# Kernel optimization log

Hardware: AMD Instinct MI355X
Metric: run time of the kernel (lower is better)

The kernel has to match this reference:

```python
import jax, jax.numpy as jnp
import numpy as np

H = 8; C = 128; P_E = 128; P_D = 64
N = 10000; E = 100000; B = 32
NEG_SLOPE = 0.01  # torch.nn.LeakyReLU default


def setup_inputs() -> dict:
    key = jax.random.key(0)
    ks = jax.random.split(key, 20)
    def lin(k, din, dout):
        return jax.random.normal(k, (din, dout), jnp.float32) / np.float32(np.sqrt(din))
    inp = dict(
        x=jax.random.normal(ks[0], (N, P_E), jnp.float32),
        index=jax.random.randint(ks[1], (2, E), 0, N),
        attr=jax.random.normal(ks[2], (E, P_D), jnp.float32),
        batch=jnp.sort(jax.random.randint(ks[3], (N,), 0, B)),
    )
    i = 4
    for l in (1, 2):
        inp[f"Wq{l}"] = lin(ks[i], P_E, H * C); i += 1
        inp[f"bq{l}"] = jnp.zeros((H * C,), jnp.float32)
        inp[f"Wk{l}"] = lin(ks[i], P_E, H * C); i += 1
        inp[f"bk{l}"] = jnp.zeros((H * C,), jnp.float32)
        inp[f"Wv{l}"] = lin(ks[i], P_E, H * C); i += 1
        inp[f"bv{l}"] = jnp.zeros((H * C,), jnp.float32)
        inp[f"We{l}"] = lin(ks[i], P_D, H * C); i += 1  # lin_edge, bias=False in PyG
        inp[f"Wskip{l}"] = lin(ks[i], P_E, P_E); i += 1  # root/skip linear (concat=False)
        inp[f"bskip{l}"] = jnp.zeros((P_E,), jnp.float32)
        inp[f"gnw{l}"] = jnp.ones((P_E,), jnp.float32)   # GraphNorm weight
        inp[f"gnb{l}"] = jnp.zeros((P_E,), jnp.float32)  # GraphNorm bias
        inp[f"gnm{l}"] = jnp.ones((P_E,), jnp.float32)   # GraphNorm mean_scale
    return inp


def transformer_conv(x, src, dst, attr, Wq, bq, Wk, bk, Wv, bv, We, Wskip, bskip):
    # PyG TransformerConv: heads=H, out_channels=C, concat=False, edge_dim=P_D,
    # dropout inactive (eval). Messages flow src=edge_index[0] -> dst=edge_index[1].
    q = (x @ Wq + bq).reshape(N, H, C)
    k = (x @ Wk + bk).reshape(N, H, C)
    v = (x @ Wv + bv).reshape(N, H, C)
    e = (attr @ We).reshape(E, H, C)
    kj = k[src] + e                                                   # [E,H,C]
    alpha = jnp.einsum('ehc,ehc->eh', q[dst], kj) / np.float32(np.sqrt(C))
    # segment softmax over destination node (numerically stable)
    amax = jax.ops.segment_max(alpha, dst, num_segments=N)            # [N,H]
    ex = jnp.exp(alpha - amax[dst])
    denom = jax.ops.segment_sum(ex, dst, num_segments=N)
    w = ex / (denom[dst] + 1e-16)                                     # [E,H]
    msg = (v[src] + e) * w[:, :, None]                                # [E,H,C]
    out = jax.ops.segment_sum(msg, dst, num_segments=N)               # [N,H,C]
    out = out.mean(axis=1)                                            # concat=False -> head mean
    return out + x @ Wskip + bskip                                    # root_weight=True


def graph_norm(x, batch, w, b, ms, eps=1e-5):
    cnt = jnp.maximum(jax.ops.segment_sum(jnp.ones((N,), x.dtype), batch, num_segments=B), 1.0)
    mean = jax.ops.segment_sum(x, batch, num_segments=B) / cnt[:, None]
    out = x - mean[batch] * ms
    var = jax.ops.segment_sum(out * out, batch, num_segments=B) / cnt[:, None]
    return out / jnp.sqrt(var[batch] + eps) * w + b


def reference(x, index, attr, batch,
              Wq1, bq1, Wk1, bk1, Wv1, bv1, We1, Wskip1, bskip1, gnw1, gnb1, gnm1,
              Wq2, bq2, Wk2, bk2, Wv2, bv2, We2, Wskip2, bskip2, gnw2, gnb2, gnm2):
    src, dst = index[0], index[1]
    h = transformer_conv(x, src, dst, attr, Wq1, bq1, Wk1, bk1, Wv1, bv1, We1, Wskip1, bskip1)
    h = jax.nn.leaky_relu(graph_norm(h, batch, gnw1, gnb1, gnm1), NEG_SLOPE)
    h = transformer_conv(h, src, dst, attr, Wq2, bq2, Wk2, bk2, Wv2, bv2, We2, Wskip2, bskip2)
    return jax.nn.leaky_relu(graph_norm(h, batch, gnw2, gnb2, gnm2), NEG_SLOPE)
```

## Files before the change

### kernel.cpp

```cpp
#include <hip/hip_runtime.h>
#include <hip/hip_bf16.h>
#include <math.h>

#define NN 10000
#define NE 100000
#define NB 32

typedef __attribute__((ext_vector_type(8))) short short8;
typedef __attribute__((ext_vector_type(4))) float f32x4;
typedef __attribute__((ext_vector_type(2))) float f32x2;
typedef _Float16 h2 __attribute__((ext_vector_type(2)));

union H8 { short8 s; h2 h[4]; };
union HU { _Float16 h; ushort u; };

__device__ inline ushort f2b(float f) {
  union { float f; unsigned u; } a; a.f = f;
  unsigned r = a.u + 0x7fff + ((a.u >> 16) & 1);
  return (ushort)(r >> 16);
}
__device__ inline float bf2f(ushort u) {
  union { unsigned u; float f; } a; a.u = ((unsigned)u) << 16;
  return a.f;
}
__device__ inline ushort f2h(float f) { HU x; x.h = (_Float16)f; return x.u; }
__device__ inline float h2f(ushort u) { HU x; x.u = u; return (float)x.h; }

__device__ inline float e4m3_sw(unsigned b) {
  unsigned s = b & 0x80, e = (b >> 3) & 15, m = b & 7;
  float v = (e == 0) ? (float)m * (1.f / 512.f) : ldexpf((float)(8 + m), (int)e - 10);
  return s ? -v : v;
}
__device__ inline unsigned f2e4m3_sw(float f) {
  unsigned s = (__float_as_uint(f) >> 24) & 0x80;
  float a = fabsf(f);
  if (a < 0.0009765625f) return s;
  if (a >= 448.f) return s | 0x7e;
  if (a < 0.015625f) {
    int q = (int)rintf(a * 512.f);
    return s | (unsigned)q;
  }
  int e2; frexpf(a, &e2);
  int sh = e2 - 4;
  int M = (int)rintf(ldexpf(a, -sh));
  if (M >= 16) { M >>= 1; sh++; }
  int E = sh + 10;
  if (E > 15) return s | 0x7e;
  return s | (unsigned)((E << 3) | (M - 8));
}

#if defined(__has_builtin)
#if __has_builtin(__builtin_amdgcn_cvt_pk_f32_fp8) && __has_builtin(__builtin_amdgcn_cvt_pk_fp8_f32)
#define HW_FP8 1
#endif
#endif

#ifdef HW_FP8
template <bool HI>
__device__ inline f32x2 dec2(unsigned w) {
  return __builtin_amdgcn_cvt_pk_f32_fp8((int)w, HI);
}
template <bool HI>
__device__ inline unsigned enc2(float a, float b, unsigned old) {
  return (unsigned)__builtin_amdgcn_cvt_pk_fp8_f32(a, b, (int)old, HI);
}
#else
template <bool HI>
__device__ inline f32x2 dec2(unsigned w) {
  unsigned x = HI ? (w >> 16) : (w & 0xffff);
  f32x2 r; r[0] = e4m3_sw(x & 0xff); r[1] = e4m3_sw((x >> 8) & 0xff);
  return r;
}
template <bool HI>
__device__ inline unsigned enc2(float a, float b, unsigned old) {
  unsigned pk = f2e4m3_sw(a) | (f2e4m3_sw(b) << 8);
  return HI ? ((old & 0xffffu) | (pk << 16)) : ((old & 0xffff0000u) | pk);
}
#endif

#if defined(__has_builtin)
#if __has_builtin(__builtin_amdgcn_fdot2)
#define FDOT2(a, b, c) __builtin_amdgcn_fdot2((a), (b), (c), false)
#endif
#endif
#ifndef FDOT2
#define FDOT2(a, b, c) ((c) + (float)(a)[0] * (float)(b)[0] + (float)(a)[1] * (float)(b)[1])
#endif

#define GLDS(g, l)                                                        \
  __builtin_amdgcn_global_load_lds(                                       \
      (const __attribute__((address_space(1))) unsigned*)(g),             \
      (__attribute__((address_space(3))) unsigned*)(l), 16, 0, 0)

__global__ __launch_bounds__(256) void k_gemm_qkvt(
    const ushort* __restrict__ Abf, const ushort* __restrict__ Bt,
    const float* __restrict__ bias, ushort* __restrict__ qt,
    unsigned char* __restrict__ kv8, int M) {
  __shared__ ushort As[128 * 128];
  __shared__ ushort Bs[128 * 128];
  const int tid = threadIdx.x;
  const int l = tid & 63, w = tid >> 6;
  const int wm = w & 1, wn = w >> 1;
  const int row0 = blockIdx.y * 128, col0 = blockIdx.x * 128;
#pragma unroll
  for (int i = 0; i < 8; ++i) {
    int idx = i * 256 + tid;
    int r = idx >> 4, cb = (idx & 15) << 4;
    int scb = cb ^ ((r & 7) << 4);
    GLDS((const char*)Abf + (size_t)(row0 + r) * 256 + scb, (char*)As + idx * 16);
    GLDS((const char*)Bt + (size_t)(col0 + r) * 256 + scb, (char*)Bs + idx * 16);
  }
  __syncthreads();
  f32x4 acc[4][4] = {};
#pragma unroll
  for (int kk = 0; kk < 4; ++kk) {
    short8 af[4], bf[4];
#pragma unroll
    for (int fm = 0; fm < 4; ++fm) {
      int r = wm * 64 + fm * 16 + (l & 15);
      int cb = (kk * 64 + ((l >> 4) << 4)) ^ ((r & 7) << 4);
      af[fm] = *(const short8*)((const char*)As + r * 256 + cb);
    }
#pragma unroll
    for (int fn = 0; fn < 4; ++fn) {
      int r = wn * 64 + fn * 16 + (l & 15);
      int cb = (kk * 64 + ((l >> 4) << 4)) ^ ((r & 7) << 4);
      bf[fn] = *(const short8*)((const char*)Bs + r * 256 + cb);
    }
#pragma unroll
    for (int fm = 0; fm < 4; ++fm)
#pragma unroll
      for (int fn = 0; fn < 4; ++fn)
        acc[fm][fn] = __builtin_amdgcn_mfma_f32_16x16x32_bf16(af[fm], bf[fn], acc[fm][fn], 0, 0, 0);
  }
  __syncthreads();
#pragma unroll
  for (int fm = 0; fm < 4; ++fm) {
    int rloc = wm * 64 + fm * 16 + ((l >> 4) << 2);
#pragma unroll
    for (int fn = 0; fn < 4; ++fn) {
      int cbyte = (wn * 64 + fn * 16 + (l & 15)) * 2;
#pragma unroll
      for (int b = 0; b < 4; ++b) {
        int r = rloc + b;
        *(ushort*)((char*)As + r * 256 + (cbyte ^ ((r & 7) << 4))) = f2h(acc[fm][fn][b]);
      }
    }
  }
  __syncthreads();
  const bool isf16 = (col0 < 1024) || (col0 >= 3072);
#pragma unroll
  for (int it = 0; it < 8; ++it) {
    int idx = it * 256 + tid;
    int r = idx >> 4, cb16 = (idx & 15) << 4;
    int gr = row0 + r;
    if (gr >= M) continue;
    short8 v = *(const short8*)((const char*)As + r * 256 + (cb16 ^ ((r & 7) << 4)));
    int co = cb16 >> 1;
    if (isf16) {
      int qc0 = ((col0 < 1024) ? col0 : (col0 - 2048)) + co;
      short8 o;
#pragma unroll
      for (int j = 0; j < 8; ++j) o[j] = (short)f2h(h2f((ushort)v[j]) + bias[col0 + co + j]);
      *(short8*)(qt + (size_t)gr * 1536 + qc0) = o;
    } else {
      float f[8];
#pragma unroll
      for (int j = 0; j < 8; ++j) f[j] = h2f((ushort)v[j]) + bias[col0 + co + j];
      unsigned w0 = 0, w1 = 0;
      w0 = enc2<false>(f[0], f[1], w0);
      w0 = enc2<true>(f[2], f[3], w0);
      w1 = enc2<false>(f[4], f[5], w1);
      w1 = enc2<true>(f[6], f[7], w1);
      uint2 st; st.x = w0; st.y = w1;
      *(uint2*)(kv8 + (size_t)gr * 2048 + (col0 - 1024) + co) = st;
    }
  }
}

__global__ __launch_bounds__(256) void k_gemm_out(
    const ushort* __restrict__ s_b, const ushort* __restrict__ xin,
    const ushort* __restrict__ W2t, const ushort* __restrict__ Wsk,
    const float* __restrict__ bsk, const float* __restrict__ mbuf,
    float* __restrict__ Cf, int M) {
  __shared__ ushort As[128 * 128];
  __shared__ ushort Bs[128 * 128];
  const int tid = threadIdx.x;
  const int l = tid & 63, w = tid >> 6;
  const int wm = w & 1, wn = w >> 1;
  const int row0 = blockIdx.y * 128;
  f32x4 acc[4][4] = {};
  for (int kt = 0; kt < 5; ++kt) {
    if (kt) __syncthreads();
    const char* Ab; const char* Bb; size_t arb, brb; int ko;
    if (kt < 4) { Ab = (const char*)s_b; arb = 1024; Bb = (const char*)W2t; brb = 1024; ko = kt * 256; }
    else        { Ab = (const char*)xin; arb = 256;  Bb = (const char*)Wsk; brb = 256;  ko = 0; }
#pragma unroll
    for (int i = 0; i < 8; ++i) {
      int idx = i * 256 + tid;
      int r = idx >> 4, cb = (idx & 15) << 4;
      int scb = cb ^ ((r & 7) << 4);
      GLDS(Ab + (size_t)(row0 + r) * arb + ko + scb, (char*)As + idx * 16);
      GLDS(Bb + (size_t)r * brb + ko + scb, (char*)Bs + idx * 16);
    }
    __syncthreads();
#pragma unroll
    for (int kk = 0; kk < 4; ++kk) {
      short8 af[4], bf[4];
#pragma unroll
      for (int fm = 0; fm < 4; ++fm) {
        int r = wm * 64 + fm * 16 + (l & 15);
        int cb = (kk * 64 + ((l >> 4) << 4)) ^ ((r & 7) << 4);
        af[fm] = *(const short8*)((const char*)As + r * 256 + cb);
      }
#pragma unroll
      for (int fn = 0; fn < 4; ++fn) {
        int r = wn * 64 + fn * 16 + (l & 15);
        int cb = (kk * 64 + ((l >> 4) << 4)) ^ ((r & 7) << 4);
        bf[fn] = *(const short8*)((const char*)Bs + r * 256 + cb);
      }
#pragma unroll
      for (int fm = 0; fm < 4; ++fm)
#pragma unroll
        for (int fn = 0; fn < 4; ++fn)
          acc[fm][fn] = __builtin_amdgcn_mfma_f32_16x16x32_bf16(af[fm], bf[fn], acc[fm][fn], 0, 0, 0);
    }
  }
#pragma unroll
  for (int fm = 0; fm < 4; ++fm) {
    int row = row0 + wm * 64 + fm * 16 + ((l >> 4) << 2);
#pragma unroll
    for (int fn = 0; fn < 4; ++fn) {
      int col = wn * 64 + fn * 16 + (l & 15);
      if (col >= 128) continue;
      float bb = bsk[col];
#pragma unroll
      for (int b = 0; b < 4; ++b) {
        int rr = row + b;
        if (rr >= M) continue;
        Cf[(size_t)rr * 128 + col] = acc[fm][fn][b] + bb + mbuf[(size_t)rr * 128 + col];
      }
    }
  }
}

struct WtPrep { const float* W[8]; ushort* O[8]; int Nc[8]; };
__global__ void k_wt_all(WtPrep P) {
  const int z = blockIdx.z;
  const int Nc = P.Nc[z];
  if ((int)blockIdx.x * 32 >= Nc) return;
  const float* __restrict__ W = P.W[z];
  ushort* __restrict__ Wt = P.O[z];
  __shared__ float tile[32][33];
  const int t = threadIdx.x, lx = t & 31, ly = t >> 5;
  const int bx = blockIdx.x, by = blockIdx.y;
#pragma unroll
  for (int i = 0; i < 4; ++i)
    tile[ly + i * 8][lx] = W[(by * 32 + ly + i * 8) * Nc + bx * 32 + lx];
  __syncthreads();
#pragma unroll
  for (int i = 0; i < 4; ++i)
    Wt[(size_t)(bx * 32 + ly + i * 8) * 128 + by * 32 + lx] = f2b(tile[lx][ly + i * 8]);
}

struct PrepPtrs {
  const float* Wq[2]; const float* We[2]; ushort* Mt[2];
  const float* bq[2]; const float* bk[2]; const float* bv[2];
  ushort* W2t[2]; float* biasAll[2];
};

__global__ __launch_bounds__(256) void k_mwt(PrepPtrs P) {
  const int L = blockIdx.y;
  const float* __restrict__ Wq = P.Wq[L];
  const float* __restrict__ We = P.We[L];
  ushort* __restrict__ Mt = P.Mt[L];
  const int h = blockIdx.x >> 3, pt = blockIdx.x & 7;
  const int t = threadIdx.x;
  __shared__ float Wes[64][129];
  __shared__ float Wqs[16][129];
#pragma unroll
  for (int i = 0; i < 32; ++i) {
    int idx = i * 256 + t;
    Wes[idx >> 7][idx & 127] = We[(idx >> 7) * 1024 + h * 128 + (idx & 127)];
  }
#pragma unroll
  for (int i = 0; i < 8; ++i) {
    int idx = i * 256 + t;
    Wqs[idx >> 7][idx & 127] = Wq[(pt * 16 + (idx >> 7)) * 1024 + h * 128 + (idx & 127)];
  }
  __syncthreads();
#pragma unroll
  for (int i = 0; i < 4; ++i) {
    int o = i * 256 + t;
    int d = o & 63, p = o >> 6;
    float s = 0.f;
#pragma unroll 8
    for (int c = 0; c < 128; ++c) s += Wqs[p][c] * Wes[d][c];
    Mt[(size_t)(h * 64 + d) * 128 + pt * 16 + p] = f2b(s);
  }
}

__global__ void k_w2t_bias(PrepPtrs P) {
  const int L = blockIdx.y;
  int o = blockIdx.x * 256 + threadIdx.x;
  if (o < 128 * 512) {
    int c = o >> 9, hd = o & 511;
    int hh = hd >> 6, d = hd & 63;
    P.W2t[L][o] = f2b(P.We[L][d * 1024 + hh * 128 + c] * 0.125f);
  } else {
    int o2 = o - 128 * 512;
    if (o2 >= 3584) return;
    if (o2 < 1024) P.biasAll[L][o2] = P.bq[L][o2];
    else if (o2 < 2048) P.biasAll[L][o2] = P.bk[L][o2 - 1024];
    else if (o2 < 3072) P.biasAll[L][o2] = P.bv[L][o2 - 2048];
    else {
      int hd = o2 - 3072;
      int h = hd >> 6, d = hd & 63;
      float s = 0.f;
      for (int c = 0; c < 128; ++c) s += P.bq[L][h * 128 + c] * P.We[L][d * 1024 + h * 128 + c];
      P.biasAll[L][o2] = s;
    }
  }
}

__global__ void k_histo_bptr(const int* __restrict__ dst, int* __restrict__ cnt,
                             const int* __restrict__ batch, int* __restrict__ bptr,
                             int nb_histo) {
  if ((int)blockIdx.x < nb_histo) {
    int e = blockIdx.x * 256 + threadIdx.x;
    if (e < NE) atomicAdd(&cnt[dst[e]], 1);
  } else {
    int b = threadIdx.x;
    if (b > NB) return;
    int lo = 0, hi = NN;
    while (lo < hi) { int mid = (lo + hi) >> 1; if (batch[mid] < b) lo = mid + 1; else hi = mid; }
    bptr[b] = lo;
  }
}

__global__ __launch_bounds__(256) void k_scan_sort(const int* __restrict__ cnt,
                                                   int* __restrict__ ptr,
                                                   int* __restrict__ order) {
  __shared__ int tsum[256];
  __shared__ int hist[256];
  __shared__ int offs[256];
  __shared__ int fill[256];
  __shared__ int sc[256];
  const int t = threadIdx.x;
  const int base = t * 40;
  int s = 0;
  for (int i = 0; i < 40; ++i) { int idx = base + i; if (idx < NN) s += cnt[idx]; }
  tsum[t] = s;
  hist[t] = 0;
  __syncthreads();
  for (int off = 1; off < 256; off <<= 1) {
    int v = (t >= off) ? tsum[t - off] : 0;
    __syncthreads();
    tsum[t] += v;
    __syncthreads();
  }
  int run = (t == 0) ? 0 : tsum[t - 1];
  for (int i = 0; i < 40; ++i) {
    int idx = base + i;
    if (idx < NN) { ptr[idx] = run; run += cnt[idx]; }
  }
  if (t == 255) ptr[NN] = tsum[255];
  for (int n = t; n < NN; n += 256) {
    int d = min(cnt[n], 255);
    atomicAdd(&hist[d], 1);
  }
  __syncthreads();
  const int rd = 255 - t;
  int v = hist[rd];
  sc[t] = v;
  __syncthreads();
  for (int off = 1; off < 256; off <<= 1) {
    int u = (t >= off) ? sc[t - off] : 0;
    __syncthreads();
    sc[t] += u;
    __syncthreads();
  }
  offs[rd] = sc[t] - v;
  fill[rd] = 0;
  __syncthreads();
  for (int n = t; n < NN; n += 256) {
    int d = min(cnt[n], 255);
    int pos = offs[d] + atomicAdd(&fill[d], 1);
    order[pos] = n;
  }
}

__global__ void k_scatter(const int* __restrict__ dst, const int* __restrict__ ptr,
                          int* __restrict__ cnt, int* __restrict__ eid) {
  int e = blockIdx.x * 256 + threadIdx.x;
  if (e < NE) {
    int d = dst[e];
    int pos = ptr[d] + atomicSub(&cnt[d], 1) - 1;
    eid[pos] = e;
  }
}

__global__ void k_permattr_cvt(const int* __restrict__ eid, const int* __restrict__ src,
                               const float* __restrict__ attr, int* __restrict__ src_p,
                               ushort* __restrict__ attr_p,
                               const float* __restrict__ x, ushort* __restrict__ xb) {
  int i = blockIdx.x * 256 + threadIdx.x;
  if (i < NE * 16) {
    int idx = i >> 4, part = i & 15;
    int e = eid[idx];
    if (part == 0) src_p[idx] = src[e];
    float4 v = *(const float4*)(attr + (size_t)e * 64 + part * 4);
    ushort4 o;
    o.x = f2h(v.x); o.y = f2h(v.y); o.z = f2h(v.z); o.w = f2h(v.w);
    *(ushort4*)(attr_p + (size_t)idx * 64 + part * 4) = o;
  } else {
    int j = i - NE * 16;
    if (j >= NN * 128 / 4) return;
    float4 v = *(const float4*)(x + j * 4);
    ushort4 o;
    o.x = f2b(v.x); o.y = f2b(v.y); o.z = f2b(v.z); o.w = f2b(v.w);
    *(ushort4*)(xb + j * 4) = o;
  }
}

__global__ __launch_bounds__(256) void k_fused(
    const ushort* __restrict__ qt, const unsigned char* __restrict__ kv8,
    const ushort* __restrict__ attr_p, const int* __restrict__ src_p,
    const int* __restrict__ ptr, const int* __restrict__ order,
    float* __restrict__ mbuf, ushort* __restrict__ s_b) {
  const int slot = blockIdx.x * 4 + (threadIdx.x >> 6);
  if (slot >= NN) return;
  const int n = order[slot];
  const int l = threadIdx.x & 63;
  const int i = l & 7;
  float qf[16];
  {
    H8 q0, q1;
    const ushort* qr = qt + (size_t)n * 1536 + l * 16;
    q0.s = *(const short8*)qr;
    q1.s = *(const short8*)(qr + 8);
#pragma unroll
    for (int j = 0; j < 8; ++j) { qf[j] = h2f((ushort)q0.s[j]); qf[8 + j] = h2f((ushort)q1.s[j]); }
  }
  H8 tv;
  tv.s = *(const short8*)(qt + (size_t)n * 1536 + 1024 + l * 8);
  const int beg = ptr[n], end = ptr[n + 1];
  float m = -1e30f, den = 0.f;
  float acc[16] = {};
  float sa[8] = {};
  uint4 kw, vw; H8 av;
  if (beg < end) {
    int s0 = src_p[beg];
    const unsigned char* kr = kv8 + (size_t)s0 * 2048 + l * 16;
    kw = *(const uint4*)kr;
    vw = *(const uint4*)(kr + 1024);
    av.s = *(const short8*)(attr_p + (size_t)beg * 64 + i * 8);
  }
  for (int idx = beg; idx < end; ++idx) {
    uint4 ckw = kw, cvw = vw; H8 cav = av;
    int nidx = (idx + 1 < end) ? idx + 1 : idx;
    int ns = src_p[nidx];
    const unsigned char* kr = kv8 + (size_t)ns * 2048 + l * 16;
    kw = *(const uint4*)kr;
    vw = *(const uint4*)(kr + 1024);
    av.s = *(const short8*)(attr_p + (size_t)nidx * 64 + i * 8);
    float p = 0.f;
    {
      const unsigned* kws = (const unsigned*)&ckw;
#pragma unroll
      for (int j = 0; j < 4; ++j) {
        f32x2 lo = dec2<false>(kws[j]), hi = dec2<true>(kws[j]);
        p += qf[4 * j] * lo[0] + qf[4 * j + 1] * lo[1]
           + qf[4 * j + 2] * hi[0] + qf[4 * j + 3] * hi[1];
      }
    }
#pragma unroll
    for (int j = 0; j < 4; ++j) p = FDOT2(tv.h[j], cav.h[j], p);
    p += __shfl_xor(p, 1, 64);
    p += __shfl_xor(p, 2, 64);
    p += __shfl_xor(p, 4, 64);
    p *= 0.12751593061420927f;
    float mn = fmaxf(m, p);
    float r = exp2f(m - mn);
    float ex = exp2f(p - mn);
    den = den * r + ex;
    {
      const unsigned* vws = (const unsigned*)&cvw;
#pragma unroll
      for (int j = 0; j < 4; ++j) {
        f32x2 lo = dec2<false>(vws[j]), hi = dec2<true>(vws[j]);
        acc[4 * j]     = acc[4 * j]     * r + ex * lo[0];
        acc[4 * j + 1] = acc[4 * j + 1] * r + ex * lo[1];
        acc[4 * j + 2] = acc[4 * j + 2] * r + ex * hi[0];
        acc[4 * j + 3] = acc[4 * j + 3] * r + ex * hi[1];
      }
    }
#pragma unroll
    for (int j = 0; j < 4; ++j) {
      sa[2 * j]     = sa[2 * j]     * r + ex * (float)cav.h[j][0];
      sa[2 * j + 1] = sa[2 * j + 1] * r + ex * (float)cav.h[j][1];
    }
    m = mn;
  }
  const float invd = den > 0.f ? 1.f / den : 0.f;
  short8 sb;
#pragma unroll
  for (int j = 0; j < 8; ++j) sb[j] = (short)f2b(sa[j] * invd);
  *(short8*)(s_b + (size_t)n * 512 + l * 8) = sb;
#pragma unroll
  for (int j = 0; j < 16; ++j) {
    float a = acc[j] * invd;
    a += __shfl_xor(a, 8, 64);
    a += __shfl_xor(a, 16, 64);
    a += __shfl_xor(a, 32, 64);
    acc[j] = a;
  }
  if (l < 8) {
    float* mb = mbuf + (size_t)n * 128 + l * 16;
#pragma unroll
    for (int j = 0; j < 16; j += 4) {
      float4 o = make_float4(acc[j] * 0.125f, acc[j + 1] * 0.125f,
                             acc[j + 2] * 0.125f, acc[j + 3] * 0.125f);
      *(float4*)(mb + j) = o;
    }
  }
}

__global__ __launch_bounds__(256) void k_gn_partial(
    const float* __restrict__ x, const int* __restrict__ bptr,
    float* __restrict__ part) {
  const int b = blockIdx.x >> 3, chunk = blockIdx.x & 7;
  const int t = threadIdx.x;
  const int c = t & 127, half = t >> 7;
  const int beg = bptr[b], end = bptr[b + 1];
  float s = 0.f, s2 = 0.f;
  for (int n = beg + chunk * 2 + half; n < end; n += 16) {
    float v = x[(size_t)n * 128 + c];
    s += v; s2 += v * v;
  }
  __shared__ float r1[256];
  __shared__ float r2[256];
  r1[t] = s; r2[t] = s2;
  __syncthreads();
  if (half == 0) {
    part[((size_t)chunk * NB + b) * 128 + c] = r1[c] + r1[c + 128];
    part[8 * NB * 128 + ((size_t)chunk * NB + b) * 128 + c] = r2[c] + r2[c + 128];
  }
}

__global__ void k_gn_apply(const float* __restrict__ x, const int* __restrict__ batch,
                           const int* __restrict__ bptr, const float* __restrict__ part,
                           const float* __restrict__ ms, const float* __restrict__ wgt,
                           const float* __restrict__ gnb,
                           float* __restrict__ fout, ushort* __restrict__ bout) {
  int i = blockIdx.x * 256 + threadIdx.x;
  int n = i >> 7, c = i & 127;
  int b = batch[n];
  float S = 0.f, S2 = 0.f;
#pragma unroll
  for (int ch = 0; ch < 8; ++ch) {
    S  += part[((size_t)ch * NB + b) * 128 + c];
    S2 += part[8 * NB * 128 + ((size_t)ch * NB + b) * 128 + c];
  }
  float cnt = fmaxf((float)(bptr[b + 1] - bptr[b]), 1.f);
  float mean = S / cnt;
  float mm = mean * ms[c];
  float var = S2 / cnt - 2.f * mm * mean + mm * mm;
  float o = (x[i] - mm) * rsqrtf(var + 1e-5f) * wgt[c] + gnb[c];
  o = o > 0.f ? o : 0.01f * o;
  if (fout) fout[i] = o;
  if (bout) bout[i] = f2b(o);
}

extern "C" void kernel_launch(void* const* d_in, const int* in_sizes, int n_in,
                              void* d_out, int out_size, void* d_ws, size_t ws_size,
                              hipStream_t stream) {
  const float* x     = (const float*)d_in[0];
  const int*   index = (const int*)d_in[1];
  const float* attr  = (const float*)d_in[2];
  const int*   batch = (const int*)d_in[3];
  const int* srcArr = index;
  const int* dstArr = index + NE;

  char* p = (char*)d_ws;
  auto take = [&](size_t bytes) {
    char* r = p;
    p += (bytes + 255) & ~(size_t)255;
    return (void*)r;
  };
  ushort* qt_b   = (ushort*)take((size_t)NN * 1536 * 2);
  unsigned char* kv8 = (unsigned char*)take((size_t)NN * 2048);
  ushort* s_b    = (ushort*)take((size_t)NN * 512 * 2);
  float*  mbuf   = (float*)take((size_t)NN * 128 * 4);
  float*  hbuf   = (float*)take((size_t)NN * 128 * 4);
  ushort* xb     = (ushort*)take((size_t)NN * 128 * 2);
  ushort* x2b    = (ushort*)take((size_t)NN * 128 * 2);
  ushort* attr_p = (ushort*)take((size_t)NE * 64 * 2);
  int*    src_p  = (int*)take((size_t)NE * 4);
  float*  part   = (float*)take((size_t)8 * NB * 128 * 2 * 4);
  int* csr_ptr   = (int*)take((size_t)(NN + 1) * 4);
  int* csr_cnt   = (int*)take((size_t)NN * 4);
  int* csr_eid   = (int*)take((size_t)NE * 4);
  int* nodeorder = (int*)take((size_t)NN * 4);
  int* bptrd     = (int*)take((size_t)(NB + 1) * 4);
  ushort* WtAll[2]; ushort* Wtsk[2]; ushort* W2t[2];
  float* biasAll[2];
  for (int L = 0; L < 2; ++L) {
    WtAll[L]   = (ushort*)take((size_t)3584 * 128 * 2);
    Wtsk[L]    = (ushort*)take((size_t)128 * 128 * 2);
    W2t[L]     = (ushort*)take((size_t)128 * 512 * 2);
    biasAll[L] = (float*)take((size_t)3584 * 4);
  }

  const int nb_histo = (NE + 255) / 256;
  hipMemsetAsync(csr_cnt, 0, NN * 4, stream);
  k_histo_bptr<<<nb_histo + 1, 256, 0, stream>>>(dstArr, csr_cnt, batch, bptrd, nb_histo);
  k_scan_sort<<<1, 256, 0, stream>>>(csr_cnt, csr_ptr, nodeorder);
  k_scatter<<<nb_histo, 256, 0, stream>>>(dstArr, csr_ptr, csr_cnt, csr_eid);
  k_permattr_cvt<<<(NE * 16 + NN * 128 / 4 + 255) / 256, 256, 0, stream>>>(
      csr_eid, srcArr, attr, src_p, attr_p, x, xb);

  WtPrep WP;
  PrepPtrs PP;
  for (int L = 0; L < 2; ++L) {
    const float* Wq  = (const float*)d_in[4 + L * 12 + 0];
    const float* bq  = (const float*)d_in[4 + L * 12 + 1];
    const float* Wk  = (const float*)d_in[4 + L * 12 + 2];
    const float* bk  = (const float*)d_in[4 + L * 12 + 3];
    const float* Wv  = (const float*)d_in[4 + L * 12 + 4];
    const float* bv  = (const float*)d_in[4 + L * 12 + 5];
    const float* We  = (const float*)d_in[4 + L * 12 + 6];
    const float* Wsk = (const float*)d_in[4 + L * 12 + 7];
    WP.W[L * 4 + 0] = Wq;  WP.O[L * 4 + 0] = WtAll[L];                      WP.Nc[L * 4 + 0] = 1024;
    WP.W[L * 4 + 1] = Wk;  WP.O[L * 4 + 1] = WtAll[L] + (size_t)1024 * 128; WP.Nc[L * 4 + 1] = 1024;
    WP.W[L * 4 + 2] = Wv;  WP.O[L * 4 + 2] = WtAll[L] + (size_t)2048 * 128; WP.Nc[L * 4 + 2] = 1024;
    WP.W[L * 4 + 3] = Wsk; WP.O[L * 4 + 3] = Wtsk[L];                       WP.Nc[L * 4 + 3] = 128;
    PP.Wq[L] = Wq; PP.We[L] = We; PP.Mt[L] = WtAll[L] + (size_t)3072 * 128;
    PP.bq[L] = bq; PP.bk[L] = bk; PP.bv[L] = bv;
    PP.W2t[L] = W2t[L]; PP.biasAll[L] = biasAll[L];
  }
  k_wt_all<<<dim3(32, 4, 8), 256, 0, stream>>>(WP);
  k_mwt<<<dim3(64, 2), 256, 0, stream>>>(PP);
  k_w2t_bias<<<dim3(270, 2), 256, 0, stream>>>(PP);

  const int MT = (NN + 127) / 128;
  for (int L = 0; L < 2; ++L) {
    const float* bsk = (const float*)d_in[4 + L * 12 + 8];
    const float* gnw = (const float*)d_in[4 + L * 12 + 9];
    const float* gnb = (const float*)d_in[4 + L * 12 + 10];
    const float* gnm = (const float*)d_in[4 + L * 12 + 11];
    const ushort* Ain = (L == 0) ? xb : x2b;

    k_gemm_qkvt<<<dim3(28, MT), 256, 0, stream>>>(Ain, WtAll[L], biasAll[L], qt_b, kv8, NN);
    k_fused<<<(NN + 3) / 4, 256, 0, stream>>>(qt_b, kv8, attr_p, src_p, csr_ptr, nodeorder, mbuf, s_b);
    k_gemm_out<<<dim3(1, MT), 256, 0, stream>>>(s_b, Ain, W2t[L], Wtsk[L], bsk, mbuf, hbuf, NN);
    k_gn_partial<<<NB * 8, 256, 0, stream>>>(hbuf, bptrd, part);
    k_gn_apply<<<NN * 128 / 256, 256, 0, stream>>>(
        hbuf, batch, bptrd, part, gnm, gnw, gnb,
        (L == 0) ? (float*)nullptr : (float*)d_out,
        (L == 0) ? x2b : (ushort*)nullptr);
  }
}
```

Before: 293.8 us.

## Fuse GraphNorm statistic reduction into output GEMM epilogue via atomics

The output GEMM epilogue now stages its 128x128 fp32 tile in shared memory and computes per-graph column sums and sums of squares, adding them to global accumulators with atomics. This removes the separate k_gn_partial kernel, along with its launch and its re-read of hbuf. The accumulators are zeroed inside the existing preprocessing kernel. In exchange, the GEMM tail gains a barrier, a shared-memory pass and atomic traffic, and summation order is no longer deterministic.

```diff
diff --git a/kernel.cpp b/kernel.cpp
--- a/kernel.cpp
+++ b/kernel.cpp
@@ -182,9 +182,12 @@
     const ushort* __restrict__ s_b, const ushort* __restrict__ xin,
     const ushort* __restrict__ W2t, const ushort* __restrict__ Wsk,
     const float* __restrict__ bsk, const float* __restrict__ mbuf,
+    const int* __restrict__ batch, const int* __restrict__ bptr,
+    float* __restrict__ gs, float* __restrict__ gs2,
     float* __restrict__ Cf, int M) {
-  __shared__ ushort As[128 * 128];
-  __shared__ ushort Bs[128 * 128];
+  __shared__ float fsm[128 * 128];
+  ushort* As = (ushort*)fsm;
+  ushort* Bs = (ushort*)fsm + 128 * 128;
   const int tid = threadIdx.x;
   const int l = tid & 63, w = tid >> 6;
   const int wm = w & 1, wn = w >> 1;
@@ -226,20 +229,43 @@
           acc[fm][fn] = __builtin_amdgcn_mfma_f32_16x16x32_bf16(af[fm], bf[fn], acc[fm][fn], 0, 0, 0);
     }
   }
+  __syncthreads();
 #pragma unroll
   for (int fm = 0; fm < 4; ++fm) {
-    int row = row0 + wm * 64 + fm * 16 + ((l >> 4) << 2);
+    int rloc0 = wm * 64 + fm * 16 + ((l >> 4) << 2);
 #pragma unroll
     for (int fn = 0; fn < 4; ++fn) {
       int col = wn * 64 + fn * 16 + (l & 15);
-      if (col >= 128) continue;
       float bb = bsk[col];
 #pragma unroll
       for (int b = 0; b < 4; ++b) {
-        int rr = row + b;
-        if (rr >= M) continue;
-        Cf[(size_t)rr * 128 + col] = acc[fm][fn][b] + bb + mbuf[(size_t)rr * 128 + col];
+        int rloc = rloc0 + b;
+        int rr = row0 + rloc;
+        float val = 0.f;
+        if (rr < M) {
+          val = acc[fm][fn][b] + bb + mbuf[(size_t)rr * 128 + col];
+          Cf[(size_t)rr * 128 + col] = val;
+        }
+        fsm[rloc * 128 + col] = val;
       }
+    }
+  }
+  __syncthreads();
+  const int c = tid & 127, half = tid >> 7;
+  const int lastr = min(row0 + 127, M - 1);
+  const int bmin = batch[row0 < M ? row0 : M - 1];
+  const int bmax = batch[lastr];
+  for (int b = bmin; b <= bmax; ++b) {
+    int rlo = max(bptr[b], row0) - row0;
+    int rhi = min(bptr[b + 1], min(row0 + 128, M)) - row0;
+    float s = 0.f, s2 = 0.f;
+    for (int r = rlo + half; r < rhi; r += 2) {
+      float v = fsm[r * 128 + c];
+      s += v; s2 += v * v;
+    }
+    if (rhi > rlo) {
+      atomicAdd(&gs[b * 128 + c], s);
+      atomicAdd(&gs2[b * 128 + c], s2);
     }
   }
 }
@@ -403,7 +429,8 @@
 __global__ void k_permattr_cvt(const int* __restrict__ eid, const int* __restrict__ src,
                                const float* __restrict__ attr, int* __restrict__ src_p,
                                ushort* __restrict__ attr_p,
-                               const float* __restrict__ x, ushort* __restrict__ xb) {
+                               const float* __restrict__ x, ushort* __restrict__ xb,
+                               float* __restrict__ gsAll) {
   int i = blockIdx.x * 256 + threadIdx.x;
   if (i < NE * 16) {
     int idx = i >> 4, part = i & 15;
@@ -413,13 +440,15 @@
     ushort4 o;
     o.x = f2h(v.x); o.y = f2h(v.y); o.z = f2h(v.z); o.w = f2h(v.w);
     *(ushort4*)(attr_p + (size_t)idx * 64 + part * 4) = o;
-  } else {
+  } else if (i < NE * 16 + NN * 128 / 4) {
     int j = i - NE * 16;
-    if (j >= NN * 128 / 4) return;
     float4 v = *(const float4*)(x + j * 4);
     ushort4 o;
     o.x = f2b(v.x); o.y = f2b(v.y); o.z = f2b(v.z); o.w = f2b(v.w);
     *(ushort4*)(xb + j * 4) = o;
+  } else {
+    int j = i - NE * 16 - NN * 128 / 4;
+    if (j < 2 * 2 * NB * 128) gsAll[j] = 0.f;
   }
 }
 
@@ -526,46 +555,19 @@
   }
 }
 
-__global__ __launch_bounds__(256) void k_gn_partial(
-    const float* __restrict__ x, const int* __restrict__ bptr,
-    float* __restrict__ part) {
-  const int b = blockIdx.x >> 3, chunk = blockIdx.x & 7;
-  const int t = threadIdx.x;
-  const int c = t & 127, half = t >> 7;
-  const int beg = bptr[b], end = bptr[b + 1];
-  float s = 0.f, s2 = 0.f;
-  for (int n = beg + chunk * 2 + half; n < end; n += 16) {
-    float v = x[(size_t)n * 128 + c];
-    s += v; s2 += v * v;
-  }
-  __shared__ float r1[256];
-  __shared__ float r2[256];
-  r1[t] = s; r2[t] = s2;
-  __syncthreads();
-  if (half == 0) {
-    part[((size_t)chunk * NB + b) * 128 + c] = r1[c] + r1[c + 128];
-    part[8 * NB * 128 + ((size_t)chunk * NB + b) * 128 + c] = r2[c] + r2[c + 128];
-  }
-}
-
 __global__ void k_gn_apply(const float* __restrict__ x, const int* __restrict__ batch,
-                           const int* __restrict__ bptr, const float* __restrict__ part,
+                           const int* __restrict__ bptr,
+                           const float* __restrict__ gs, const float* __restrict__ gs2,
                            const float* __restrict__ ms, const float* __restrict__ wgt,
                            const float* __restrict__ gnb,
                            float* __restrict__ fout, ushort* __restrict__ bout) {
   int i = blockIdx.x * 256 + threadIdx.x;
   int n = i >> 7, c = i & 127;
   int b = batch[n];
-  float S = 0.f, S2 = 0.f;
-#pragma unroll
-  for (int ch = 0; ch < 8; ++ch) {
-    S  += part[((size_t)ch * NB + b) * 128 + c];
-    S2 += part[8 * NB * 128 + ((size_t)ch * NB + b) * 128 + c];
-  }
   float cnt = fmaxf((float)(bptr[b + 1] - bptr[b]), 1.f);
-  float mean = S / cnt;
+  float mean = gs[b * 128 + c] / cnt;
   float mm = mean * ms[c];
-  float var = S2 / cnt - 2.f * mm * mean + mm * mm;
+  float var = gs2[b * 128 + c] / cnt - 2.f * mm * mean + mm * mm;
   float o = (x[i] - mm) * rsqrtf(var + 1e-5f) * wgt[c] + gnb[c];
   o = o > 0.f ? o : 0.01f * o;
   if (fout) fout[i] = o;
@@ -597,7 +599,7 @@
   ushort* x2b    = (ushort*)take((size_t)NN * 128 * 2);
   ushort* attr_p = (ushort*)take((size_t)NE * 64 * 2);
   int*    src_p  = (int*)take((size_t)NE * 4);
-  float*  part   = (float*)take((size_t)8 * NB * 128 * 2 * 4);
+  float*  gsAll  = (float*)take((size_t)2 * 2 * NB * 128 * 4);
   int* csr_ptr   = (int*)take((size_t)(NN + 1) * 4);
   int* csr_cnt   = (int*)take((size_t)NN * 4);
   int* csr_eid   = (int*)take((size_t)NE * 4);
@@ -617,8 +619,8 @@
   k_histo_bptr<<<nb_histo + 1, 256, 0, stream>>>(dstArr, csr_cnt, batch, bptrd, nb_histo);
   k_scan_sort<<<1, 256, 0, stream>>>(csr_cnt, csr_ptr, nodeorder);
   k_scatter<<<nb_histo, 256, 0, stream>>>(dstArr, csr_ptr, csr_cnt, csr_eid);
-  k_permattr_cvt<<<(NE * 16 + NN * 128 / 4 + 255) / 256, 256, 0, stream>>>(
-      csr_eid, srcArr, attr, src_p, attr_p, x, xb);
+  k_permattr_cvt<<<(NE * 16 + NN * 128 / 4 + 2 * 2 * NB * 128 + 255) / 256, 256, 0, stream>>>(
+      csr_eid, srcArr, attr, src_p, attr_p, x, xb, gsAll);
 
   WtPrep WP;
   PrepPtrs PP;
@@ -650,13 +652,15 @@
     const float* gnb = (const float*)d_in[4 + L * 12 + 10];
     const float* gnm = (const float*)d_in[4 + L * 12 + 11];
     const ushort* Ain = (L == 0) ? xb : x2b;
+    float* gs  = gsAll + (size_t)L * 2 * NB * 128;
+    float* gs2 = gs + NB * 128;
 
     k_gemm_qkvt<<<dim3(28, MT), 256, 0, stream>>>(Ain, WtAll[L], biasAll[L], qt_b, kv8, NN);
     k_fused<<<(NN + 3) / 4, 256, 0, stream>>>(qt_b, kv8, attr_p, src_p, csr_ptr, nodeorder, mbuf, s_b);
-    k_gemm_out<<<dim3(1, MT), 256, 0, stream>>>(s_b, Ain, W2t[L], Wtsk[L], bsk, mbuf, hbuf, NN);
-    k_gn_partial<<<NB * 8, 256, 0, stream>>>(hbuf, bptrd, part);
+    k_gemm_out<<<dim3(1, MT), 256, 0, stream>>>(
+        s_b, Ain, W2t[L], Wtsk[L], bsk, mbuf, batch, bptrd, gs, gs2, hbuf, NN);
     k_gn_apply<<<NN * 128 / 256, 256, 0, stream>>>(
-        hbuf, batch, bptrd, part, gnm, gnw, gnb,
+        hbuf, batch, bptrd, gs, gs2, gnm, gnw, gnb,
         (L == 0) ? (float*)nullptr : (float*)d_out,
         (L == 0) ? x2b : (ushort*)nullptr);
   }
```

Result: faster. 278.1 us (-5.4%).
